# Kernel tuning notes

Measured on AMD Instinct MI355X. Metric: run time of the kernel, lower is better.

## Reference

```python
import jax, jax.numpy as jnp
import numpy as np

N, D, P, Q = 4096, 512, 8, 32
MARGIN = 1.0
L2_WEIGHT = 0.005
EPS = 1e-6  # torch.nn.PairwiseDistance default eps, added to the difference


def setup_inputs() -> dict:
    key = jax.random.key(0)
    k1, k2, k3 = jax.random.split(key, 3)
    batch = jax.random.normal(k1, (N, D), dtype=jnp.float32)
    anchors = jnp.arange(N, dtype=jnp.int64) if jax.config.jax_enable_x64 else jnp.arange(N, dtype=jnp.int32)
    pos_idx = jax.random.randint(k2, (N, P), 0, N)
    neg_idx = jax.random.randint(k3, (N, Q), 0, N)
    return {"batch": batch, "anchors": anchors, "pos_idx": pos_idx, "neg_idx": neg_idx}


def reference(batch, anchors, pos_idx, neg_idx):
    # batch: [N, D]; anchors: [N]; pos_idx: [N, P]; neg_idx: [N, Q]
    a = batch[anchors]                       # [N, D]
    # PairwiseDistance(p=2): (sum |x - y + eps|^2)^(1/2)
    d_pos = jnp.sqrt(jnp.sum((a[:, None, :] - batch[pos_idx] + EPS) ** 2, axis=-1))  # [N, P]
    d_neg = jnp.sqrt(jnp.sum((a[:, None, :] - batch[neg_idx] + EPS) ** 2, axis=-1))  # [N, Q]
    pos_term = jax.scipy.special.logsumexp(d_pos, axis=1)            # [N]
    neg_term = jax.scipy.special.logsumexp(MARGIN - d_neg, axis=1)   # [N]
    per_anchor = jax.nn.relu(pos_term + neg_term)                    # [N]
    l2_term = L2_WEIGHT * jnp.mean(jnp.sqrt(jnp.sum(batch ** 2, axis=1)))
    return jnp.mean(per_anchor) + l2_term
```

## Files before the change

### kernel.cpp

```cpp
#include <hip/hip_runtime.h>
#include <hip/hip_fp8.h>
#include <math.h>
#include <float.h>

#define NN 4096
#define DD 512
#define PP 8
#define QQ 32
#define NB_TOT 40
#define NPW 10
constexpr float MARGIN = 1.0f;
constexpr float L2W    = 0.005f;
constexpr float EPS    = 1e-6f;

#define WS_NORM (NN * 128)
#define WS_RES  (WS_NORM + NN)

__device__ inline float wave_reduce_sum(float v) {
    v += __shfl_xor(v, 32, 64);
    v += __shfl_xor(v, 16, 64);
    v += __shfl_xor(v,  8, 64);
    v += __shfl_xor(v,  4, 64);
    v += __shfl_xor(v,  2, 64);
    v += __shfl_xor(v,  1, 64);
    return v;
}

__device__ inline float wave_reduce_max(float v) {
    v = fmaxf(v, __shfl_xor(v, 32, 64));
    v = fmaxf(v, __shfl_xor(v, 16, 64));
    v = fmaxf(v, __shfl_xor(v,  8, 64));
    v = fmaxf(v, __shfl_xor(v,  4, 64));
    v = fmaxf(v, __shfl_xor(v,  2, 64));
    v = fmaxf(v, __shfl_xor(v,  1, 64));
    return v;
}

__device__ inline float half_reduce_sum(float v) {
    v += __shfl_xor(v, 16, 64);
    v += __shfl_xor(v,  8, 64);
    v += __shfl_xor(v,  4, 64);
    v += __shfl_xor(v,  2, 64);
    v += __shfl_xor(v,  1, 64);
    return v;
}

__global__ __launch_bounds__(256) void convert_kernel(
    const float4* __restrict__ batch4,
    uint2*        __restrict__ fb,
    float*        __restrict__ norms)
{
    const int row  = blockIdx.x * 4 + (threadIdx.x >> 6);
    const int lane = threadIdx.x & 63;

    const float4 v0 = batch4[row * 128 + lane * 2];
    const float4 v1 = batch4[row * 128 + lane * 2 + 1];

    union { unsigned char b[8]; uint2 u; } pk;
    pk.b[0] = __hip_fp8_e4m3(v0.x).__x;
    pk.b[1] = __hip_fp8_e4m3(v0.y).__x;
    pk.b[2] = __hip_fp8_e4m3(v0.z).__x;
    pk.b[3] = __hip_fp8_e4m3(v0.w).__x;
    pk.b[4] = __hip_fp8_e4m3(v1.x).__x;
    pk.b[5] = __hip_fp8_e4m3(v1.y).__x;
    pk.b[6] = __hip_fp8_e4m3(v1.z).__x;
    pk.b[7] = __hip_fp8_e4m3(v1.w).__x;
    fb[row * 64 + lane] = pk.u;

    float s = v0.x*v0.x + v0.y*v0.y + v0.z*v0.z + v0.w*v0.w
            + v1.x*v1.x + v1.y*v1.y + v1.z*v1.z + v1.w*v1.w;
    s = wave_reduce_sum(s);
    if (lane == 0) norms[row] = sqrtf(s);
}

__device__ inline void decode16(const uint4 q, float* f) {
    union { uint4 u; unsigned char c[16]; } v; v.u = q;
    #pragma unroll
    for (int j = 0; j < 16; ++j) {
        __hip_fp8_e4m3 h; h.__x = v.c[j];
        f[j] = (float)h;
    }
}

__global__ __launch_bounds__(256) void dist_kernel(
    const uint4* __restrict__ fb,
    const int*   __restrict__ anchors,
    const int*   __restrict__ pos_idx,
    const int*   __restrict__ neg_idx,
    const float* __restrict__ norms,
    float*       __restrict__ res)
{
    const int i    = blockIdx.x;
    const int tid  = threadIdx.x;
    const int lane = tid & 63;
    const int wave = tid >> 6;
    const int half = lane >> 5;
    const int l32  = lane & 31;
    const int jb   = wave * NPW;

    __shared__ float dist[NB_TOT];

    const int arow = anchors[i];
    const uint4 ahq = fb[(size_t)arow * 32 + l32];
    float a[16];
    decode16(ahq, a);
    #pragma unroll
    for (int k = 0; k < 16; ++k) a[k] += EPS;

    int idxs[NPW];
    #pragma unroll
    for (int t = 0; t < NPW; ++t) {
        const int j = jb + t;
        idxs[t] = (j < PP) ? pos_idx[i * PP + j] : neg_idx[i * QQ + (j - PP)];
    }

    uint4 bq[5];
    #pragma unroll
    for (int t = 0; t < 5; ++t)
        bq[t] = fb[(size_t)idxs[2 * t + half] * 32 + l32];
    __builtin_amdgcn_sched_barrier(0);

    float s[5];
    #pragma unroll
    for (int t = 0; t < 5; ++t) {
        float b[16];
        decode16(bq[t], b);
        float acc = 0.0f;
        #pragma unroll
        for (int k = 0; k < 16; ++k) {
            const float d = a[k] - b[k];
            acc = fmaf(d, d, acc);
        }
        s[t] = acc;
    }

    #pragma unroll
    for (int t = 0; t < 5; ++t) s[t] = half_reduce_sum(s[t]);

    #pragma unroll
    for (int t = 0; t < 5; ++t)
        if (l32 == 0) dist[jb + 2 * t + half] = sqrtf(s[t]);

    __syncthreads();

    if (wave == 0) {
        const float d = (lane < NB_TOT) ? dist[lane] : 0.0f;

        const bool pact = (lane < PP);
        const float pm = wave_reduce_max(pact ? d : -FLT_MAX);
        const float ps = wave_reduce_sum(pact ? expf(d - pm) : 0.0f);
        const float pos_term = pm + logf(ps);

        const bool nact = (lane >= PP) && (lane < NB_TOT);
        const float nv = MARGIN - d;
        const float nm = wave_reduce_max(nact ? nv : -FLT_MAX);
        const float ns = wave_reduce_sum(nact ? expf(nv - nm) : 0.0f);
        const float neg_term = nm + logf(ns);

        if (lane == 0)
            res[i] = fmaxf(0.0f, pos_term + neg_term) + L2W * norms[i];
    }
}

__global__ __launch_bounds__(256) void reduce_kernel(
    const float* __restrict__ res, float* __restrict__ out)
{
    const int tid  = threadIdx.x;
    const int lane = tid & 63;
    const int wave = tid >> 6;

    const float4* __restrict__ w4 = reinterpret_cast<const float4*>(res);
    float s = 0.0f;
    #pragma unroll
    for (int k = 0; k < 4; ++k) {
        const float4 v = w4[tid + 256 * k];
        s += v.x + v.y + v.z + v.w;
    }
    s = wave_reduce_sum(s);

    __shared__ float part[4];
    if (lane == 0) part[wave] = s;
    __syncthreads();
    if (tid == 0)
        out[0] = (part[0] + part[1] + part[2] + part[3]) * (1.0f / (float)NN);
}

extern "C" void kernel_launch(void* const* d_in, const int* in_sizes, int n_in,
                              void* d_out, int out_size, void* d_ws, size_t ws_size,
                              hipStream_t stream) {
    const float* batch   = (const float*)d_in[0];
    const int*   anchors = (const int*)d_in[1];
    const int*   pos_idx = (const int*)d_in[2];
    const int*   neg_idx = (const int*)d_in[3];
    float*       wsf     = (float*)d_ws;
    float*       out     = (float*)d_out;

    uint2* fb    = (uint2*)wsf;
    float* norms = wsf + WS_NORM;
    float* res   = wsf + WS_RES;

    convert_kernel<<<NN / 4, 256, 0, stream>>>((const float4*)batch, fb, norms);
    dist_kernel<<<NN, 256, 0, stream>>>((const uint4*)fb, anchors, pos_idx,
                                        neg_idx, norms, res);
    reduce_kernel<<<1, 256, 0, stream>>>(res, out);
}
```

Measured before the change: 82.33 us.

## Use hardware packed FP8 conversions and fold final mean into atomic adds

Replaces the per-byte software FP8 encode and decode with the packed hardware conversion builtins in both the convert and distance kernels. It also removes the separate reduce kernel: the convert kernel zeroes the output, and each distance block atomically adds its scaled per-anchor loss. This saves one kernel launch and many conversion instructions. In exchange it adds 4096 atomics to one address and makes the summation order nondeterministic.

```diff
diff --git a/kernel.cpp b/kernel.cpp
--- a/kernel.cpp
+++ b/kernel.cpp
@@ -1,5 +1,4 @@
 #include <hip/hip_runtime.h>
-#include <hip/hip_fp8.h>
 #include <math.h>
 #include <float.h>
 
@@ -13,8 +12,9 @@
 constexpr float L2W    = 0.005f;
 constexpr float EPS    = 1e-6f;
 
+typedef float floatx2 __attribute__((ext_vector_type(2)));
+
 #define WS_NORM (NN * 128)
-#define WS_RES  (WS_NORM + NN)
 
 __device__ inline float wave_reduce_sum(float v) {
     v += __shfl_xor(v, 32, 64);
@@ -48,7 +48,8 @@
 __global__ __launch_bounds__(256) void convert_kernel(
     const float4* __restrict__ batch4,
     uint2*        __restrict__ fb,
-    float*        __restrict__ norms)
+    float*        __restrict__ norms,
+    float*        __restrict__ out)
 {
     const int row  = blockIdx.x * 4 + (threadIdx.x >> 6);
     const int lane = threadIdx.x & 63;
@@ -56,29 +57,29 @@
     const float4 v0 = batch4[row * 128 + lane * 2];
     const float4 v1 = batch4[row * 128 + lane * 2 + 1];
 
-    union { unsigned char b[8]; uint2 u; } pk;
-    pk.b[0] = __hip_fp8_e4m3(v0.x).__x;
-    pk.b[1] = __hip_fp8_e4m3(v0.y).__x;
-    pk.b[2] = __hip_fp8_e4m3(v0.z).__x;
-    pk.b[3] = __hip_fp8_e4m3(v0.w).__x;
-    pk.b[4] = __hip_fp8_e4m3(v1.x).__x;
-    pk.b[5] = __hip_fp8_e4m3(v1.y).__x;
-    pk.b[6] = __hip_fp8_e4m3(v1.z).__x;
-    pk.b[7] = __hip_fp8_e4m3(v1.w).__x;
-    fb[row * 64 + lane] = pk.u;
+    int w0 = 0, w1 = 0;
+    w0 = __builtin_amdgcn_cvt_pk_fp8_f32(v0.x, v0.y, w0, false);
+    w0 = __builtin_amdgcn_cvt_pk_fp8_f32(v0.z, v0.w, w0, true);
+    w1 = __builtin_amdgcn_cvt_pk_fp8_f32(v1.x, v1.y, w1, false);
+    w1 = __builtin_amdgcn_cvt_pk_fp8_f32(v1.z, v1.w, w1, true);
+    uint2 pk; pk.x = (unsigned)w0; pk.y = (unsigned)w1;
+    fb[row * 64 + lane] = pk;
 
     float s = v0.x*v0.x + v0.y*v0.y + v0.z*v0.z + v0.w*v0.w
             + v1.x*v1.x + v1.y*v1.y + v1.z*v1.z + v1.w*v1.w;
     s = wave_reduce_sum(s);
     if (lane == 0) norms[row] = sqrtf(s);
+    if (blockIdx.x == 0 && threadIdx.x == 0) out[0] = 0.0f;
 }
 
 __device__ inline void decode16(const uint4 q, float* f) {
-    union { uint4 u; unsigned char c[16]; } v; v.u = q;
+    const int w[4] = { (int)q.x, (int)q.y, (int)q.z, (int)q.w };
     #pragma unroll
-    for (int j = 0; j < 16; ++j) {
-        __hip_fp8_e4m3 h; h.__x = v.c[j];
-        f[j] = (float)h;
+    for (int j = 0; j < 4; ++j) {
+        const floatx2 lo = __builtin_amdgcn_cvt_pk_f32_fp8(w[j], false);
+        const floatx2 hi = __builtin_amdgcn_cvt_pk_f32_fp8(w[j], true);
+        f[j * 4 + 0] = lo[0]; f[j * 4 + 1] = lo[1];
+        f[j * 4 + 2] = hi[0]; f[j * 4 + 3] = hi[1];
     }
 }
 
@@ -88,7 +89,7 @@
     const int*   __restrict__ pos_idx,
     const int*   __restrict__ neg_idx,
     const float* __restrict__ norms,
-    float*       __restrict__ res)
+    float*       __restrict__ out)
 {
     const int i    = blockIdx.x;
     const int tid  = threadIdx.x;
@@ -157,32 +158,11 @@
         const float ns = wave_reduce_sum(nact ? expf(nv - nm) : 0.0f);
         const float neg_term = nm + logf(ns);
 
-        if (lane == 0)
-            res[i] = fmaxf(0.0f, pos_term + neg_term) + L2W * norms[i];
+        if (lane == 0) {
+            const float val = fmaxf(0.0f, pos_term + neg_term) + L2W * norms[i];
+            atomicAdd(out, val * (1.0f / (float)NN));
+        }
     }
-}
-
-__global__ __launch_bounds__(256) void reduce_kernel(
-    const float* __restrict__ res, float* __restrict__ out)
-{
-    const int tid  = threadIdx.x;
-    const int lane = tid & 63;
-    const int wave = tid >> 6;
-
-    const float4* __restrict__ w4 = reinterpret_cast<const float4*>(res);
-    float s = 0.0f;
-    #pragma unroll
-    for (int k = 0; k < 4; ++k) {
-        const float4 v = w4[tid + 256 * k];
-        s += v.x + v.y + v.z + v.w;
-    }
-    s = wave_reduce_sum(s);
-
-    __shared__ float part[4];
-    if (lane == 0) part[wave] = s;
-    __syncthreads();
-    if (tid == 0)
-        out[0] = (part[0] + part[1] + part[2] + part[3]) * (1.0f / (float)NN);
 }
 
 extern "C" void kernel_launch(void* const* d_in, const int* in_sizes, int n_in,
@@ -197,10 +177,8 @@
 
     uint2* fb    = (uint2*)wsf;
     float* norms = wsf + WS_NORM;
-    float* res   = wsf + WS_RES;
 
-    convert_kernel<<<NN / 4, 256, 0, stream>>>((const float4*)batch, fb, norms);
+    convert_kernel<<<NN / 4, 256, 0, stream>>>((const float4*)batch, fb, norms, out);
     dist_kernel<<<NN, 256, 0, stream>>>((const uint4*)fb, anchors, pos_idx,
-                                        neg_idx, norms, res);
-    reduce_kernel<<<1, 256, 0, stream>>>(res, out);
+                                        neg_idx, norms, out);
 }
```

Result: slower. 119.4 us (+45.0%).
